# Optimization experiments

Measured on AMD Instinct MI355X. Metric: run time of the kernel, lower is better.

## Reference

```python
import jax, jax.numpy as jnp
import numpy as np

ENC_HID = 256
DEC_HID = 256
BATCH = 64
SRC_LEN = 4096


def setup_inputs() -> dict:
    key = jax.random.key(0)
    k1, k2, k3, k4, k5 = jax.random.split(key, 5)
    hidden = jax.random.normal(k1, (1, BATCH, DEC_HID), dtype=jnp.float32)
    encoder_outputs = jax.random.normal(k2, (SRC_LEN, BATCH, 2 * ENC_HID), dtype=jnp.float32)
    # nn.Linear(2*enc_hid + dec_hid, dec_hid): weight [out, in], bias [out]
    W = jax.random.normal(k3, (DEC_HID, 2 * ENC_HID + DEC_HID), dtype=jnp.float32) * 0.02
    b = jax.random.normal(k4, (DEC_HID,), dtype=jnp.float32) * 0.02
    v = jax.random.uniform(k5, (DEC_HID,), dtype=jnp.float32)
    return {"hidden": hidden, "encoder_outputs": encoder_outputs, "W": W, "b": b, "v": v}


def reference(hidden, encoder_outputs, W, b, v):
    # hidden: [n_layers, B, D] -> take first layer: [B, D]
    h = hidden[0]
    # encoder_outputs: [S, B, 2E] -> [B, S, 2E]
    eo = jnp.transpose(encoder_outputs, (1, 0, 2))
    D = h.shape[-1]
    # Split the concat+linear: cat is (hidden, encoder_outputs) along last dim,
    # so W = [Wh | We] along its input axis. Mathematically identical to
    # tanh(attn(cat(h_rep, eo))) but avoids materializing the concat.
    Wh, We = W[:, :D], W[:, D:]
    # energy: [B, S, D]
    energy = jnp.tanh(jnp.einsum('bd,kd->bk', h, Wh)[:, None, :]
                      + jnp.einsum('bse,ke->bsk', eo, We)
                      + b)
    # scores: [B, S]  (v . energy, same as bmm(v[1,D], energy[D,S]))
    scores = jnp.einsum('bsk,k->bs', energy, v)
    return jax.nn.softmax(scores, axis=1)
```

## Files before the change

kernel.cpp:

```cpp
#include <hip/hip_runtime.h>
#include <stdint.h>

#define ENC2   512
#define NDIM   256
#define BATCH  64
#define SLEN   4096
#define NROWS  (SLEN*BATCH)
#define BLKR   128
#define NKB    16

typedef _Float16 half8 __attribute__((ext_vector_type(8)));
typedef float    f32x4 __attribute__((ext_vector_type(4)));

__device__ __forceinline__ float tanh_fast(float x) {
  float e = __expf(2.0f * x);
  return 1.0f - 2.0f * __builtin_amdgcn_rcpf(e + 1.0f);
}

__device__ __forceinline__ void gld_lds16(const _Float16* g, _Float16* l) {
  __builtin_amdgcn_global_load_lds(
      (const __attribute__((address_space(1))) void*)g,
      (__attribute__((address_space(3))) void*)l, 16, 0, 0);
}

__global__ __launch_bounds__(256) void pack_We(const float* __restrict__ W,
                                               _Float16* __restrict__ wp) {
  int t = blockIdx.x * 256 + threadIdx.x;
  int lane = t & 63;
  int ct   = (t >> 6) & 15;
  int kb   = t >> 10;
  int c  = ct * 16 + (lane & 15);
  int kk = kb * 32 + (lane >> 4) * 8;
  const float* src = W + (size_t)c * 768 + 256 + kk;
  half8 h;
#pragma unroll
  for (int j = 0; j < 8; ++j) h[j] = (_Float16)src[j];
  *(half8*)(wp + (size_t)t * 8) = h;
}

__global__ __launch_bounds__(256) void compute_hb(const float* __restrict__ hidden,
                                                  const float* __restrict__ W,
                                                  const float* __restrict__ bvec,
                                                  float* __restrict__ hb) {
  __shared__ float hs[256];
  int b = blockIdx.x, k = threadIdx.x;
  hs[k] = hidden[b * 256 + k];
  __syncthreads();
  const float* wr = W + (size_t)k * 768;
  float acc = bvec[k];
#pragma unroll 8
  for (int d = 0; d < 256; d += 4) {
    f32x4 wv = *(const f32x4*)(wr + d);
    acc += wv[0]*hs[d] + wv[1]*hs[d+1] + wv[2]*hs[d+2] + wv[3]*hs[d+3];
  }
  hb[b * 256 + k] = acc;
}

__global__ __launch_bounds__(256) void attn_energy(const float* __restrict__ eo,
                                                   const _Float16* __restrict__ wp,
                                                   const float* __restrict__ hb,
                                                   const float* __restrict__ v,
                                                   float* __restrict__ scores) {
  __shared__ _Float16 lds[2][8192];
  const int tid  = threadIdx.x;
  const int w    = tid >> 6;
  const int lane = tid & 63;
  const int g    = lane >> 4;
  const int l15  = lane & 15;
  const int rowbase = blockIdx.x * BLKR + w * 32;

  const float* aptr0 = eo + (size_t)(rowbase + l15) * ENC2 + g * 8;
  const float* aptr1 = aptr0 + 16 * ENC2;

  f32x4 acc[2][16];
#pragma unroll
  for (int i = 0; i < 2; ++i)
#pragma unroll
    for (int j = 0; j < 16; ++j) acc[i][j] = (f32x4){0.f, 0.f, 0.f, 0.f};

  {
    const _Float16* src = wp + (size_t)(w * 4) * 512 + lane * 8;
    _Float16* dst = &lds[0][(w * 4) * 512];
#pragma unroll
    for (int i = 0; i < 4; ++i) gld_lds16(src + i * 512, dst + i * 512);
  }
  f32x4 ar00 = *(const f32x4*)(aptr0);
  f32x4 ar01 = *(const f32x4*)(aptr0 + 4);
  f32x4 ar10 = *(const f32x4*)(aptr1);
  f32x4 ar11 = *(const f32x4*)(aptr1 + 4);
  __syncthreads();

  int cur = 0;
#pragma unroll 1
  for (int kb = 0; kb < NKB; ++kb) {
    half8 a0, a1;
#pragma unroll
    for (int j = 0; j < 4; ++j) {
      a0[j]     = (_Float16)ar00[j];
      a0[j + 4] = (_Float16)ar01[j];
      a1[j]     = (_Float16)ar10[j];
      a1[j + 4] = (_Float16)ar11[j];
    }
    if (kb < NKB - 1) {
      const _Float16* src = wp + (size_t)(kb + 1) * 8192 + (w * 4) * 512 + lane * 8;
      _Float16* dst = &lds[cur ^ 1][(w * 4) * 512];
#pragma unroll
      for (int i = 0; i < 4; ++i) gld_lds16(src + i * 512, dst + i * 512);
      const float* p0 = aptr0 + (size_t)(kb + 1) * 32;
      const float* p1 = aptr1 + (size_t)(kb + 1) * 32;
      ar00 = *(const f32x4*)(p0);
      ar01 = *(const f32x4*)(p0 + 4);
      ar10 = *(const f32x4*)(p1);
      ar11 = *(const f32x4*)(p1 + 4);
    }
    const _Float16* bufc = &lds[cur][lane * 8];
#pragma unroll
    for (int ct = 0; ct < 16; ++ct) {
      half8 bf = *(const half8*)(bufc + ct * 512);
      acc[0][ct] = __builtin_amdgcn_mfma_f32_16x16x32_f16(a0, bf, acc[0][ct], 0, 0, 0);
      acc[1][ct] = __builtin_amdgcn_mfma_f32_16x16x32_f16(a1, bf, acc[1][ct], 0, 0, 0);
    }
    __syncthreads();
    cur ^= 1;
  }

  float sc0[4] = {0.f, 0.f, 0.f, 0.f};
  float sc1[4] = {0.f, 0.f, 0.f, 0.f};
#pragma unroll
  for (int ct = 0; ct < 16; ++ct) {
    int k = ct * 16 + l15;
    float vk = v[k];
    const float* hbk = hb + k;
#pragma unroll
    for (int r = 0; r < 4; ++r) {
      int b0 = (rowbase + g * 4 + r) & 63;
      int b1 = (rowbase + 16 + g * 4 + r) & 63;
      sc0[r] += vk * tanh_fast(acc[0][ct][r] + hbk[(size_t)b0 * 256]);
      sc1[r] += vk * tanh_fast(acc[1][ct][r] + hbk[(size_t)b1 * 256]);
    }
  }
#pragma unroll
  for (int m = 1; m < 16; m <<= 1) {
#pragma unroll
    for (int r = 0; r < 4; ++r) {
      sc0[r] += __shfl_xor(sc0[r], m, 64);
      sc1[r] += __shfl_xor(sc1[r], m, 64);
    }
  }
  int r = l15;
  if (r < 4) {
    float o0 = (r == 0) ? sc0[0] : (r == 1) ? sc0[1] : (r == 2) ? sc0[2] : sc0[3];
    float o1 = (r == 0) ? sc1[0] : (r == 1) ? sc1[1] : (r == 2) ? sc1[2] : sc1[3];
    int gr0 = rowbase + g * 4 + r;
    int gr1 = rowbase + 16 + g * 4 + r;
    scores[(size_t)(gr0 & 63) * SLEN + (gr0 >> 6)] = o0;
    scores[(size_t)(gr1 & 63) * SLEN + (gr1 >> 6)] = o1;
  }
}

__global__ __launch_bounds__(256) void softmax_rows(const float* __restrict__ scores,
                                                    float* __restrict__ out) {
  int b = blockIdx.x, t = threadIdx.x;
  const f32x4* in4 = (const f32x4*)(scores + (size_t)b * SLEN);
  f32x4* out4 = (f32x4*)(out + (size_t)b * SLEN);
  f32x4 x0 = in4[t], x1 = in4[256 + t], x2 = in4[512 + t], x3 = in4[768 + t];
  float m = fmaxf(fmaxf(fmaxf(x0[0], x0[1]), fmaxf(x0[2], x0[3])),
                  fmaxf(fmaxf(x1[0], x1[1]), fmaxf(x1[2], x1[3])));
  m = fmaxf(m, fmaxf(fmaxf(fmaxf(x2[0], x2[1]), fmaxf(x2[2], x2[3])),
                     fmaxf(fmaxf(x3[0], x3[1]), fmaxf(x3[2], x3[3]))));
#pragma unroll
  for (int off = 1; off < 64; off <<= 1) m = fmaxf(m, __shfl_xor(m, off, 64));
  __shared__ float redm[4], reds[4];
  int w = t >> 6, lane = t & 63;
  if (lane == 0) redm[w] = m;
  __syncthreads();
  m = fmaxf(fmaxf(redm[0], redm[1]), fmaxf(redm[2], redm[3]));
  float s = 0.f;
#pragma unroll
  for (int j = 0; j < 4; ++j) { x0[j] = __expf(x0[j] - m); s += x0[j]; }
#pragma unroll
  for (int j = 0; j < 4; ++j) { x1[j] = __expf(x1[j] - m); s += x1[j]; }
#pragma unroll
  for (int j = 0; j < 4; ++j) { x2[j] = __expf(x2[j] - m); s += x2[j]; }
#pragma unroll
  for (int j = 0; j < 4; ++j) { x3[j] = __expf(x3[j] - m); s += x3[j]; }
#pragma unroll
  for (int off = 1; off < 64; off <<= 1) s += __shfl_xor(s, off, 64);
  if (lane == 0) reds[w] = s;
  __syncthreads();
  s = (reds[0] + reds[1]) + (reds[2] + reds[3]);
  float inv = 1.0f / s;
#pragma unroll
  for (int j = 0; j < 4; ++j) { x0[j] *= inv; x1[j] *= inv; x2[j] *= inv; x3[j] *= inv; }
  out4[t] = x0; out4[256 + t] = x1; out4[512 + t] = x2; out4[768 + t] = x3;
}

extern "C" void kernel_launch(void* const* d_in, const int* in_sizes, int n_in,
                              void* d_out, int out_size, void* d_ws, size_t ws_size,
                              hipStream_t stream) {
  (void)in_sizes; (void)n_in; (void)out_size; (void)ws_size;
  const float* hidden = (const float*)d_in[0];
  const float* eo     = (const float*)d_in[1];
  const float* W      = (const float*)d_in[2];
  const float* bvec   = (const float*)d_in[3];
  const float* v      = (const float*)d_in[4];
  float* out = (float*)d_out;

  uint8_t* ws = (uint8_t*)d_ws;
  _Float16* wp  = (_Float16*)ws;
  float* hb     = (float*)(ws + 262144);
  float* scores = (float*)(ws + 262144 + 65536);

  pack_We<<<64, 256, 0, stream>>>(W, wp);
  compute_hb<<<64, 256, 0, stream>>>(hidden, W, bvec, hb);
  attn_energy<<<NROWS / BLKR, 256, 0, stream>>>(eo, wp, hb, v, scores);
  softmax_rows<<<BATCH, 256, 0, stream>>>(scores, out);
}
```

Baseline: 763.7 us.

## Load packed We straight from global/L2 instead of LDS, prefetch A two steps ahead

Drops the LDS double-buffer for the packed fp16 weight matrix and its per-iteration __syncthreads. Each wave now reads its B fragments directly from global memory, relying on L1/L2 because every block reuses the same 256 KB weight. A-operand loads from encoder_outputs are prefetched two k-steps ahead, and the kernel asks for two blocks per CU through launch bounds. This removes barrier stalls and LDS traffic at the cost of more global/L1 weight loads and more register pressure.

```diff
diff --git a/kernel.cpp b/kernel.cpp
--- a/kernel.cpp
+++ b/kernel.cpp
@@ -15,12 +15,6 @@
 __device__ __forceinline__ float tanh_fast(float x) {
   float e = __expf(2.0f * x);
   return 1.0f - 2.0f * __builtin_amdgcn_rcpf(e + 1.0f);
-}
-
-__device__ __forceinline__ void gld_lds16(const _Float16* g, _Float16* l) {
-  __builtin_amdgcn_global_load_lds(
-      (const __attribute__((address_space(1))) void*)g,
-      (__attribute__((address_space(3))) void*)l, 16, 0, 0);
 }
 
 __global__ __launch_bounds__(256) void pack_We(const float* __restrict__ W,
@@ -56,12 +50,11 @@
   hb[b * 256 + k] = acc;
 }
 
-__global__ __launch_bounds__(256) void attn_energy(const float* __restrict__ eo,
-                                                   const _Float16* __restrict__ wp,
-                                                   const float* __restrict__ hb,
-                                                   const float* __restrict__ v,
-                                                   float* __restrict__ scores) {
-  __shared__ _Float16 lds[2][8192];
+__global__ __launch_bounds__(256, 2) void attn_energy(const float* __restrict__ eo,
+                                                      const _Float16* __restrict__ wp,
+                                                      const float* __restrict__ hb,
+                                                      const float* __restrict__ v,
+                                                      float* __restrict__ scores) {
   const int tid  = threadIdx.x;
   const int w    = tid >> 6;
   const int lane = tid & 63;
@@ -78,51 +71,61 @@
 #pragma unroll
     for (int j = 0; j < 16; ++j) acc[i][j] = (f32x4){0.f, 0.f, 0.f, 0.f};
 
-  {
-    const _Float16* src = wp + (size_t)(w * 4) * 512 + lane * 8;
-    _Float16* dst = &lds[0][(w * 4) * 512];
-#pragma unroll
-    for (int i = 0; i < 4; ++i) gld_lds16(src + i * 512, dst + i * 512);
-  }
-  f32x4 ar00 = *(const f32x4*)(aptr0);
-  f32x4 ar01 = *(const f32x4*)(aptr0 + 4);
-  f32x4 ar10 = *(const f32x4*)(aptr1);
-  f32x4 ar11 = *(const f32x4*)(aptr1 + 4);
-  __syncthreads();
-
-  int cur = 0;
+#define LDA(v00, v01, v10, v11, KB)                                  \
+  do {                                                               \
+    const float* p0_ = aptr0 + (size_t)(KB) * 32;                    \
+    const float* p1_ = aptr1 + (size_t)(KB) * 32;                    \
+    v00 = *(const f32x4*)(p0_);                                      \
+    v01 = *(const f32x4*)(p0_ + 4);                                  \
+    v10 = *(const f32x4*)(p1_);                                      \
+    v11 = *(const f32x4*)(p1_ + 4);                                  \
+  } while (0)
+
+#define CVT(a0, a1, v00, v01, v10, v11)                              \
+  do {                                                               \
+    _Pragma("unroll")                                                \
+    for (int j = 0; j < 4; ++j) {                                    \
+      a0[j] = (_Float16)v00[j]; a0[j + 4] = (_Float16)v01[j];        \
+      a1[j] = (_Float16)v10[j]; a1[j + 4] = (_Float16)v11[j];        \
+    }                                                                \
+  } while (0)
+
+  f32x4 x00, x01, x10, x11;
+  f32x4 y00, y01, y10, y11;
+  LDA(x00, x01, x10, x11, 0);
+  LDA(y00, y01, y10, y11, 1);
+
+  const half8* bp = (const half8*)wp + lane;
+
 #pragma unroll 1
-  for (int kb = 0; kb < NKB; ++kb) {
-    half8 a0, a1;
-#pragma unroll
-    for (int j = 0; j < 4; ++j) {
-      a0[j]     = (_Float16)ar00[j];
-      a0[j + 4] = (_Float16)ar01[j];
-      a1[j]     = (_Float16)ar10[j];
-      a1[j + 4] = (_Float16)ar11[j];
-    }
-    if (kb < NKB - 1) {
-      const _Float16* src = wp + (size_t)(kb + 1) * 8192 + (w * 4) * 512 + lane * 8;
-      _Float16* dst = &lds[cur ^ 1][(w * 4) * 512];
-#pragma unroll
-      for (int i = 0; i < 4; ++i) gld_lds16(src + i * 512, dst + i * 512);
-      const float* p0 = aptr0 + (size_t)(kb + 1) * 32;
-      const float* p1 = aptr1 + (size_t)(kb + 1) * 32;
-      ar00 = *(const f32x4*)(p0);
-      ar01 = *(const f32x4*)(p0 + 4);
-      ar10 = *(const f32x4*)(p1);
-      ar11 = *(const f32x4*)(p1 + 4);
-    }
-    const _Float16* bufc = &lds[cur][lane * 8];
-#pragma unroll
-    for (int ct = 0; ct < 16; ++ct) {
-      half8 bf = *(const half8*)(bufc + ct * 512);
-      acc[0][ct] = __builtin_amdgcn_mfma_f32_16x16x32_f16(a0, bf, acc[0][ct], 0, 0, 0);
-      acc[1][ct] = __builtin_amdgcn_mfma_f32_16x16x32_f16(a1, bf, acc[1][ct], 0, 0, 0);
-    }
-    __syncthreads();
-    cur ^= 1;
-  }
+  for (int kb = 0; kb < NKB; kb += 2) {
+    {
+      half8 a0, a1;
+      CVT(a0, a1, x00, x01, x10, x11);
+      if (kb + 2 < NKB) LDA(x00, x01, x10, x11, kb + 2);
+      const half8* bpc = bp + (size_t)(kb * 16) * 64;
+#pragma unroll
+      for (int ct = 0; ct < 16; ++ct) {
+        half8 bf = bpc[(size_t)ct * 64];
+        acc[0][ct] = __builtin_amdgcn_mfma_f32_16x16x32_f16(a0, bf, acc[0][ct], 0, 0, 0);
+        acc[1][ct] = __builtin_amdgcn_mfma_f32_16x16x32_f16(a1, bf, acc[1][ct], 0, 0, 0);
+      }
+    }
+    {
+      half8 a0, a1;
+      CVT(a0, a1, y00, y01, y10, y11);
+      if (kb + 3 < NKB) LDA(y00, y01, y10, y11, kb + 3);
+      const half8* bpc = bp + (size_t)((kb + 1) * 16) * 64;
+#pragma unroll
+      for (int ct = 0; ct < 16; ++ct) {
+        half8 bf = bpc[(size_t)ct * 64];
+        acc[0][ct] = __builtin_amdgcn_mfma_f32_16x16x32_f16(a0, bf, acc[0][ct], 0, 0, 0);
+        acc[1][ct] = __builtin_amdgcn_mfma_f32_16x16x32_f16(a1, bf, acc[1][ct], 0, 0, 0);
+      }
+    }
+  }
+#undef LDA
+#undef CVT
 
   float sc0[4] = {0.f, 0.f, 0.f, 0.f};
   float sc1[4] = {0.f, 0.f, 0.f, 0.f};
```

After: 778.3 us. No clear change (+1.9%).
